# Optimization experiments

Hardware: AMD Instinct MI355X
Metric: run time of the kernel (lower is better)

## Reference

```python
import jax, jax.numpy as jnp
import numpy as np

N = 96        # num_nodes
D = 64        # emb_size / n_hid
BS = 16
T = 13
G = 1         # num_graph

# all N^2 ordered pairs, receiver-major: edge e=i*N+j has receiver i, sender j
_REC = jnp.repeat(jnp.arange(N), N)
_SEND = jnp.tile(jnp.arange(N), N)


def _lin(shape, key, scale=0.05):
    return (jax.random.normal(key, shape, dtype=jnp.float32) * scale)


def setup_inputs() -> dict:
    key = jax.random.key(0)
    ks = jax.random.split(key, 24)
    inp = {
        "skill_seq": jax.random.randint(ks[0], (BS, T), 0, N, dtype=jnp.int32),
        "adj": jax.random.uniform(ks[1], (G, BS, N, N), dtype=jnp.float32),
        "node_embeddings": jax.random.normal(ks[2], (G, N, D), dtype=jnp.float32),
        # edge MLP
        "W_msg1": _lin((2 * D, D), ks[3]), "b_msg1": jnp.zeros((D,), jnp.float32),
        "W_msg2": _lin((D, D), ks[4]),     "b_msg2": jnp.zeros((D,), jnp.float32),
        # GRU hidden projections (no bias)
        "W_hr": _lin((D, D), ks[5]), "W_hi": _lin((D, D), ks[6]), "W_hh": _lin((D, D), ks[7]),
        # GRU input projections (bias)
        "W_ir": _lin((D, D), ks[8]),  "b_ir": jnp.zeros((D,), jnp.float32),
        "W_ii": _lin((D, D), ks[9]),  "b_ii": jnp.zeros((D,), jnp.float32),
        "W_in": _lin((D, D), ks[10]), "b_in": jnp.zeros((D,), jnp.float32),
        # output MLP
        "W_o1": _lin((D, D), ks[11]), "b_o1": jnp.zeros((D,), jnp.float32),
        "W_o2": _lin((D, D), ks[12]), "b_o2": jnp.zeros((D,), jnp.float32),
        "W_o3": _lin((D, D), ks[13]), "b_o3": jnp.zeros((D,), jnp.float32),
    }
    return inp


def _forward(skill_seq, adj, node_embeddings,
             W_msg1, b_msg1, W_msg2, b_msg2,
             W_hr, W_hi, W_hh,
             W_ir, b_ir, W_ii, b_ii, W_in, b_in,
             W_o1, b_o1, W_o2, b_o2, W_o3, b_o3):
    bs, time_steps = skill_seq.shape
    hidden0 = jnp.zeros((G, bs, N, D), dtype=adj.dtype)
    emb = node_embeddings[0]  # [N, D] (num_graph=1)

    def step(hidden, skill_t):
        # gather senders/receivers over the node axis -> [G, bs, N^2, 2D]
        senders = hidden[:, :, _SEND, :]
        receivers = hidden[:, :, _REC, :]
        pre_msg = jnp.concatenate([senders, receivers], axis=-1)
        msg = jnp.tanh(pre_msg @ W_msg1 + b_msg1)        # [G, bs, N^2, D]
        msg = jnp.tanh(msg @ W_msg2 + b_msg2)
        msg = msg.reshape(G, bs, N, N, D)                # receiver i, sender j
        # mask by adjacency and scatter-sum over senders, then /N
        agg = jnp.einsum('gbij,gbijd->gbid', adj, msg) / N   # [G, bs, N, D]
        inputs = emb[skill_t][None, :, None, :]          # [1, bs, 1, D]
        r = jax.nn.sigmoid(inputs @ W_ir + b_ir + agg @ W_hr)
        i = jax.nn.sigmoid(inputs @ W_ii + b_ii + agg @ W_hi)
        n = jnp.tanh(inputs @ W_in + b_in + r * (agg @ W_hh))
        hidden = (1.0 - i) * n + i * hidden
        pred = jax.nn.relu(hidden @ W_o1 + b_o1)
        pred = jax.nn.relu(pred @ W_o2 + b_o2)
        pred = pred @ W_o3 + b_o3                        # [G, bs, N, D]
        return hidden, pred

    skills_t = skill_seq[:, :time_steps - 1].T           # [T-1, bs]
    _, preds = jax.lax.scan(step, hidden0, skills_t)     # [T-1, G, bs, N, D]
    # torch: stack(dim=1) -> [G, T-1, bs, N, D]; transpose(1,2) -> [G, bs, T-1, N, D]
    return jnp.transpose(preds, (1, 2, 0, 3, 4))


def reference(skill_seq, adj, node_embeddings,
              W_msg1, b_msg1, W_msg2, b_msg2,
              W_hr, W_hi, W_hh,
              W_ir, b_ir, W_ii, b_ii, W_in, b_in,
              W_o1, b_o1, W_o2, b_o2, W_o3, b_o3):
    return _forward(skill_seq, adj, node_embeddings,
                    W_msg1, b_msg1, W_msg2, b_msg2,
                    W_hr, W_hi, W_hh,
                    W_ir, b_ir, W_ii, b_ii, W_in, b_in,
                    W_o1, b_o1, W_o2, b_o2, W_o3, b_o3)
```

## Files before the change

### kernel.cpp

```cpp
#include <hip/hip_runtime.h>

typedef unsigned short ushort_t;
typedef __attribute__((ext_vector_type(8))) short short8;
typedef __attribute__((ext_vector_type(4))) float floatx4;

#define NN 96
#define DD 64
#define BSZ 16
#define TSTEP 12
#define JSPLIT 8
#define JPW 12
#define ITILES 6

#define OFF_HALL  0u
#define OFF_S     5111808u
#define OFF_R     5505024u
#define OFF_E     5898240u
#define OFF_PART  5971968u
#define OFF_WSWZ  9117696u
#define HSLOT     98304

static __device__ __forceinline__ short f2bf(float f){
    union { float f; unsigned u; } v; v.f = f;
    unsigned u = v.u;
    u += 0x7fffu + ((u >> 16) & 1u);
    return (short)(u >> 16);
}
static __device__ __forceinline__ float fast_tanh(float x){
    x = fminf(20.f, fmaxf(-20.f, x));
    float p = __expf(2.f * x);
    return (p - 1.f) * __builtin_amdgcn_rcpf(p + 1.f);
}
static __device__ __forceinline__ float fast_sigmoid(float x){
    x = fminf(30.f, fmaxf(-30.f, x));
    float p = __expf(-x);
    return __builtin_amdgcn_rcpf(1.f + p);
}
static __device__ __forceinline__ void zero4(floatx4* a){
    floatx4 z = {0.f,0.f,0.f,0.f};
    a[0]=z; a[1]=z; a[2]=z; a[3]=z;
}
static __device__ __forceinline__ void buildA(const float* sM, int col, int quad, short8& a0, short8& a1){
    floatx4 f0 = *(const floatx4*)&sM[col*68 + quad*8];
    floatx4 f1 = *(const floatx4*)&sM[col*68 + quad*8 + 4];
    floatx4 f2 = *(const floatx4*)&sM[col*68 + 32 + quad*8];
    floatx4 f3 = *(const floatx4*)&sM[col*68 + 32 + quad*8 + 4];
    #pragma unroll
    for (int jj = 0; jj < 4; jj++){
        a0[jj]   = f2bf(f0[jj]);
        a0[4+jj] = f2bf(f1[jj]);
        a1[jj]   = f2bf(f2[jj]);
        a1[4+jj] = f2bf(f3[jj]);
    }
}
static __device__ __forceinline__ void mm16(short8 a0, short8 a1, const short8* wzm, int l, floatx4* acc){
    #pragma unroll
    for (int nt = 0; nt < 4; nt++){
        short8 b0 = wzm[nt*64 + l];
        short8 b1 = wzm[(4 + nt)*64 + l];
        acc[nt] = __builtin_amdgcn_mfma_f32_16x16x32_bf16(a0, b0, acc[nt], 0, 0, 0);
        acc[nt] = __builtin_amdgcn_mfma_f32_16x16x32_bf16(a1, b1, acc[nt], 0, 0, 0);
    }
}
static __device__ __forceinline__ void mm16r(short8 a0, short8 a1, const short8* f, floatx4* acc){
    #pragma unroll
    for (int nt = 0; nt < 4; nt++){
        acc[nt] = __builtin_amdgcn_mfma_f32_16x16x32_bf16(a0, f[nt],     acc[nt], 0, 0, 0);
        acc[nt] = __builtin_amdgcn_mfma_f32_16x16x32_bf16(a1, f[4 + nt], acc[nt], 0, 0, 0);
    }
}

__global__ __launch_bounds__(256) void k_init(
    const float* __restrict__ emb, const float* __restrict__ Wmsg1,
    const float* __restrict__ Wmsg2,
    const float* __restrict__ Whr, const float* __restrict__ Whi, const float* __restrict__ Whh,
    const float* __restrict__ Wir, const float* __restrict__ bir,
    const float* __restrict__ Wii, const float* __restrict__ bii,
    const float* __restrict__ Win, const float* __restrict__ bin,
    const float* __restrict__ Wo1, const float* __restrict__ Wo2, const float* __restrict__ Wo3,
    float* __restrict__ hz, float* __restrict__ SRz,
    float* __restrict__ Ef, ushort_t* __restrict__ wswz)
{
    int wg = blockIdx.x, tid = threadIdx.x;
    if (wg < 288) {
        int flat = wg*256 + tid;
        floatx4 z = {0.f,0.f,0.f,0.f};
        if (flat < 24576) ((floatx4*)hz)[flat] = z;
        else              ((floatx4*)SRz)[flat - 24576] = z;
    } else if (wg < 360) {
        int flat = (wg - 288)*256 + tid;
        int m = flat / 6144; int r = flat % 6144; int s = r >> 6; int d = r & 63;
        const float* W = (m==0)? Wir : (m==1)? Wii : Win;
        const float* B = (m==0)? bir : (m==1)? bii : bin;
        float acc = B[d];
        #pragma unroll 8
        for (int k = 0; k < 64; k++)
            acc += emb[s*64 + k] * W[k*64 + d];
        Ef[flat] = acc;
    } else {
        int flat = (wg - 360)*256 + tid;
        int m = flat >> 12; int q = flat & 4095;
        int jj = q & 7, lane = (q >> 3) & 63, nt = (q >> 9) & 3, kc = q >> 11;
        int k = kc*32 + ((lane >> 4) << 3) + jj;
        int n = nt*16 + (lane & 15);
        const float* src; int idx = k*64 + n;
        switch (m) {
          case 0: src = Wmsg2; break;
          case 1: src = Whr;  break;
          case 2: src = Whi;  break;
          case 3: src = Whh;  break;
          case 4: src = Wmsg1; break;
          case 5: src = Wmsg1; idx = (64 + k)*64 + n; break;
          case 6: src = Wo1; break;
          case 7: src = Wo2; break;
          default: src = Wo3; break;
        }
        wswz[flat] = (ushort_t)f2bf(src[idx]);
    }
}

__global__ __launch_bounds__(256) void k_msg(
    const float* __restrict__ adj, const float* __restrict__ b1in, const float* __restrict__ b2in,
    const float* __restrict__ Sg, const float* __restrict__ Rg,
    const ushort_t* __restrict__ wswz, float* __restrict__ partial)
{
    __shared__ float sS[JPW*64];
    __shared__ float sRB[16*68];
    __shared__ float sAdj[16*JPW];
    __shared__ float sAgg[4][16*68];
    int wg = blockIdx.x;
    int js = wg / 96; int rem = wg % 96; int b = rem / 6; int it = rem % 6;
    int tid = threadIdx.x; int w = tid >> 6; int l = tid & 63;
    int quad = l >> 4, col = l & 15;
    int j0 = js * JPW;

    for (int q = tid; q < JPW*16; q += 256) {
        int row = q >> 4, c4 = (q & 15) * 4;
        *(floatx4*)&sS[row*64 + c4] = *(const floatx4*)&Sg[(b*NN + j0 + row)*64 + c4];
    }
    for (int q = tid; q < 16*16; q += 256) {
        int row = q >> 4, c4 = (q & 15) * 4;
        floatx4 r4 = *(const floatx4*)&Rg[(b*NN + it*16 + row)*64 + c4];
        floatx4 b4 = *(const floatx4*)&b1in[c4];
        floatx4 o = r4 + b4;
        *(floatx4*)&sRB[row*68 + c4] = o;
    }
    for (int q = tid; q < 16*JPW; q += 256) {
        int i = q / JPW, j = q % JPW;
        sAdj[q] = adj[(b*NN + it*16 + i)*NN + j0 + j];
    }
    const short8* wz = (const short8*)wswz;
    short8 w2f[2][4];
    #pragma unroll
    for (int kc = 0; kc < 2; kc++)
      #pragma unroll
      for (int nt = 0; nt < 4; nt++)
        w2f[kc][nt] = wz[(kc*4 + nt)*64 + l];
    float b2v[4];
    #pragma unroll
    for (int nt = 0; nt < 4; nt++) b2v[nt] = b2in[nt*16 + col];
    __syncthreads();

    float rbv[16];
    #pragma unroll
    for (int c = 0; c < 4; c++)
        *(floatx4*)&rbv[c*4] = *(const floatx4*)&sRB[col*68 + (c>>1)*32 + quad*8 + (c&1)*4];

    float agg[4][4];
    #pragma unroll
    for (int nt=0;nt<4;nt++)
      #pragma unroll
      for (int r=0;r<4;r++) agg[nt][r] = 0.f;

    for (int c = 0; c < 3; c++) {
        int jl = w*3 + c;
        float sv[16];
        #pragma unroll
        for (int cc = 0; cc < 4; cc++)
            *(floatx4*)&sv[cc*4] = *(const floatx4*)&sS[jl*64 + (cc>>1)*32 + quad*8 + (cc&1)*4];
        short8 a0, a1;
        #pragma unroll
        for (int e = 0; e < 8; e++) {
            a0[e] = f2bf(fast_tanh(sv[e]   + rbv[e]));
            a1[e] = f2bf(fast_tanh(sv[8+e] + rbv[8+e]));
        }
        floatx4 acc[4];
        zero4(acc);
        #pragma unroll
        for (int nt = 0; nt < 4; nt++) {
            acc[nt] = __builtin_amdgcn_mfma_f32_16x16x32_bf16(a0, w2f[0][nt], acc[nt], 0,0,0);
            acc[nt] = __builtin_amdgcn_mfma_f32_16x16x32_bf16(a1, w2f[1][nt], acc[nt], 0,0,0);
        }
        float adjv[4];
        #pragma unroll
        for (int r = 0; r < 4; r++) adjv[r] = sAdj[(quad*4 + r)*JPW + jl];
        #pragma unroll
        for (int nt = 0; nt < 4; nt++)
          #pragma unroll
          for (int r = 0; r < 4; r++)
            agg[nt][r] += adjv[r] * fast_tanh(acc[nt][r] + b2v[nt]);
    }
    #pragma unroll
    for (int nt = 0; nt < 4; nt++)
      #pragma unroll
      for (int r = 0; r < 4; r++)
        sAgg[w][(quad*4 + r)*68 + nt*16 + col] = agg[nt][r];
    __syncthreads();
    {
        int i = tid >> 4, k4 = (tid & 15) * 4;
        floatx4 s0 = *(const floatx4*)&sAgg[0][i*68 + k4];
        floatx4 s1 = *(const floatx4*)&sAgg[1][i*68 + k4];
        floatx4 s2 = *(const floatx4*)&sAgg[2][i*68 + k4];
        floatx4 s3 = *(const floatx4*)&sAgg[3][i*68 + k4];
        floatx4 o = (s0 + s1) + (s2 + s3);
        o = o * (1.f/96.f);
        *(floatx4*)&partial[((js*BSZ + b)*NN + it*16 + i)*64 + k4] = o;
    }
}

__global__ __launch_bounds__(256) void k_gru(
    const int* __restrict__ skills, const float* __restrict__ partial,
    const float* __restrict__ Ef, const ushort_t* __restrict__ wswz,
    const float* __restrict__ hprev, float* __restrict__ hcur,
    float* __restrict__ Sg, float* __restrict__ Rg, int t)
{
    __shared__ float sM[16*68];
    __shared__ float sG[3][16*68];
    __shared__ float sH[16*64];
    __shared__ float sE[3][64];
    int wg = blockIdx.x; int b = wg / 6, it = wg % 6;
    int tid = threadIdx.x; int w = tid >> 6; int l = tid & 63;
    int quad = l >> 4, col = l & 15;
    int i = tid >> 4, k4 = (tid & 15) * 4;

    const short8* wzb = (const short8*)wswz;
    short8 fG[8], fSR[8];
    if (w < 3) {
        #pragma unroll
        for (int q = 0; q < 8; q++) fG[q] = wzb[(1 + w)*512 + q*64 + l];
    }
    if (w < 2) {
        #pragma unroll
        for (int q = 0; q < 8; q++) fSR[q] = wzb[(4 + w)*512 + q*64 + l];
    }

    {
        floatx4 a = {0.f,0.f,0.f,0.f};
        #pragma unroll
        for (int p = 0; p < JSPLIT; p++)
            a += *(const floatx4*)&partial[((p*BSZ + b)*NN + it*16 + i)*64 + k4];
        *(floatx4*)&sM[i*68 + k4] = a;
        *(floatx4*)&sH[i*64 + k4] = *(const floatx4*)&hprev[(b*NN + it*16 + i)*64 + k4];
    }
    if (tid < 192) {
        int s = skills[b*13 + t];
        ((float*)sE)[tid] = Ef[(tid >> 6)*6144 + s*64 + (tid & 63)];
    }
    __syncthreads();

    if (w < 3) {
        short8 a0, a1;
        buildA(sM, col, quad, a0, a1);
        floatx4 acc[4];
        zero4(acc);
        mm16r(a0, a1, fG, acc);
        #pragma unroll
        for (int nt = 0; nt < 4; nt++)
          #pragma unroll
          for (int r = 0; r < 4; r++)
            sG[w][(quad*4 + r)*68 + nt*16 + col] = acc[nt][r];
    }
    __syncthreads();

    {
        float h[4];
        #pragma unroll
        for (int e = 0; e < 4; e++) {
            int d = k4 + e;
            float gr = fast_sigmoid(sE[0][d] + sG[0][i*68 + d]);
            float gi = fast_sigmoid(sE[1][d] + sG[1][i*68 + d]);
            float nv = fast_tanh(sE[2][d] + gr * sG[2][i*68 + d]);
            h[e] = (1.f - gi)*nv + gi*sH[i*64 + d];
        }
        #pragma unroll
        for (int e = 0; e < 4; e++) sM[i*68 + k4 + e] = h[e];
        floatx4 hv = { h[0], h[1], h[2], h[3] };
        *(floatx4*)&hcur[(b*NN + it*16 + i)*64 + k4] = hv;
    }
    __syncthreads();

    if (w < 2) {
        short8 a0, a1;
        buildA(sM, col, quad, a0, a1);
        floatx4 acc[4];
        zero4(acc);
        mm16r(a0, a1, fSR, acc);
        float* dst = (w == 0) ? Sg : Rg;
        #pragma unroll
        for (int nt = 0; nt < 4; nt++)
          #pragma unroll
          for (int r = 0; r < 4; r++)
            dst[(b*NN + it*16 + quad*4 + r)*64 + nt*16 + col] = acc[nt][r];
    }
}

__global__ __launch_bounds__(256) void k_out(
    const float* __restrict__ hall, const ushort_t* __restrict__ wswz,
    const float* __restrict__ bo1, const float* __restrict__ bo2, const float* __restrict__ bo3,
    float* __restrict__ out)
{
    __shared__ float sT[4][16*68];
    int tid = threadIdx.x; int w = tid >> 6; int l = tid & 63;
    int quad = l >> 4, col = l & 15;
    int g = blockIdx.x*4 + w;
    int ts = g / 96; int rem = g % 96; int b = rem / 6, it = rem % 6;
    const float* hsrc = hall + (size_t)(ts + 1)*HSLOT + (b*NN + it*16)*64;
    float* sm = sT[w];
    {
        int i = l >> 2, c0 = (l & 3) * 16;
        #pragma unroll
        for (int cc = 0; cc < 4; cc++)
            *(floatx4*)&sm[i*68 + c0 + cc*4] = *(const floatx4*)&hsrc[i*64 + c0 + cc*4];
    }
    float bv1[4], bv2[4], bv3[4];
    #pragma unroll
    for (int nt = 0; nt < 4; nt++) {
        bv1[nt] = bo1[nt*16 + col];
        bv2[nt] = bo2[nt*16 + col];
        bv3[nt] = bo3[nt*16 + col];
    }
    short8 a0, a1;
    floatx4 acc[4];

    buildA(sm, col, quad, a0, a1);
    zero4(acc);
    mm16(a0, a1, (const short8*)wswz + 6*512, l, acc);
    #pragma unroll
    for (int nt = 0; nt < 4; nt++)
      #pragma unroll
      for (int r = 0; r < 4; r++)
        sm[(quad*4 + r)*68 + nt*16 + col] = fmaxf(0.f, acc[nt][r] + bv1[nt]);

    buildA(sm, col, quad, a0, a1);
    zero4(acc);
    mm16(a0, a1, (const short8*)wswz + 7*512, l, acc);
    #pragma unroll
    for (int nt = 0; nt < 4; nt++)
      #pragma unroll
      for (int r = 0; r < 4; r++)
        sm[(quad*4 + r)*68 + nt*16 + col] = fmaxf(0.f, acc[nt][r] + bv2[nt]);

    buildA(sm, col, quad, a0, a1);
    zero4(acc);
    mm16(a0, a1, (const short8*)wswz + 8*512, l, acc);
    #pragma unroll
    for (int nt = 0; nt < 4; nt++)
      #pragma unroll
      for (int r = 0; r < 4; r++)
        out[((b*TSTEP + ts)*NN + it*16 + quad*4 + r)*64 + nt*16 + col] = acc[nt][r] + bv3[nt];
}

extern "C" void kernel_launch(void* const* d_in, const int* in_sizes, int n_in,
                              void* d_out, int out_size, void* d_ws, size_t ws_size,
                              hipStream_t stream) {
    const int*   skills = (const int*)d_in[0];
    const float* adj    = (const float*)d_in[1];
    const float* emb    = (const float*)d_in[2];
    const float* Wmsg1  = (const float*)d_in[3];
    const float* b1     = (const float*)d_in[4];
    const float* Wmsg2  = (const float*)d_in[5];
    const float* b2     = (const float*)d_in[6];
    const float* Whr    = (const float*)d_in[7];
    const float* Whi    = (const float*)d_in[8];
    const float* Whh    = (const float*)d_in[9];
    const float* Wir    = (const float*)d_in[10];
    const float* bir    = (const float*)d_in[11];
    const float* Wii    = (const float*)d_in[12];
    const float* bii    = (const float*)d_in[13];
    const float* Win    = (const float*)d_in[14];
    const float* bin    = (const float*)d_in[15];
    const float* Wo1    = (const float*)d_in[16];
    const float* bo1    = (const float*)d_in[17];
    const float* Wo2    = (const float*)d_in[18];
    const float* bo2    = (const float*)d_in[19];
    const float* Wo3    = (const float*)d_in[20];
    const float* bo3    = (const float*)d_in[21];

    char* ws = (char*)d_ws;
    float*    hall    = (float*)(ws + OFF_HALL);
    float*    Sg      = (float*)(ws + OFF_S);
    float*    Rg      = (float*)(ws + OFF_R);
    float*    Ef      = (float*)(ws + OFF_E);
    float*    partial = (float*)(ws + OFF_PART);
    ushort_t* wswz    = (ushort_t*)(ws + OFF_WSWZ);
    float*    out     = (float*)d_out;

    k_init<<<dim3(504), dim3(256), 0, stream>>>(emb, Wmsg1, Wmsg2, Whr, Whi, Whh,
        Wir, bir, Wii, bii, Win, bin, Wo1, Wo2, Wo3, hall, Sg, Ef, wswz);

    for (int t = 0; t < TSTEP; t++) {
        k_msg<<<dim3(JSPLIT*BSZ*ITILES), dim3(256), 0, stream>>>(adj, b1, b2, Sg, Rg, wswz, partial);
        k_gru<<<dim3(BSZ*ITILES), dim3(256), 0, stream>>>(skills, partial, Ef, wswz,
            hall + (size_t)t*HSLOT, hall + (size_t)(t+1)*HSLOT, Sg, Rg, t);
    }
    k_out<<<dim3(288), dim3(256), 0, stream>>>(hall, wswz, bo1, bo2, bo3, out);
}
```

Measured before the change: 273.5 us.

## Fuse final GRU step into output kernel, rebalance msg split, use native bf16 casts

The last timestep's GRU update now runs inside k_out for the final slot, which removes one k_gru launch and its dependent h write/read. The message kernel's j-split goes from 8 to 12 with 8 senders per workgroup, and its inner loop is fully unrolled, trading more partial-sum traffic for more parallel workgroups. Manual float-to-bf16 rounding is replaced by native __bf16 conversions, and the clamps in tanh and sigmoid are dropped. Removing the clamps risks inf/NaN for large arguments, because the exp-based formulas can overflow to inf/inf.

```diff
diff --git a/kernel.cpp b/kernel.cpp
--- a/kernel.cpp
+++ b/kernel.cpp
@@ -2,14 +2,15 @@
 
 typedef unsigned short ushort_t;
 typedef __attribute__((ext_vector_type(8))) short short8;
+typedef __attribute__((ext_vector_type(8))) __bf16 bf16x8;
 typedef __attribute__((ext_vector_type(4))) float floatx4;
 
 #define NN 96
 #define DD 64
 #define BSZ 16
 #define TSTEP 12
-#define JSPLIT 8
-#define JPW 12
+#define JSPLIT 12
+#define JPW 8
 #define ITILES 6
 
 #define OFF_HALL  0u
@@ -17,8 +18,10 @@
 #define OFF_R     5505024u
 #define OFF_E     5898240u
 #define OFF_PART  5971968u
-#define OFF_WSWZ  9117696u
+#define OFF_WSWZ  10690560u
 #define HSLOT     98304
+
+union fragU { short8 s; bf16x8 b; };
 
 static __device__ __forceinline__ short f2bf(float f){
     union { float f; unsigned u; } v; v.f = f;
@@ -27,12 +30,10 @@
     return (short)(u >> 16);
 }
 static __device__ __forceinline__ float fast_tanh(float x){
-    x = fminf(20.f, fmaxf(-20.f, x));
     float p = __expf(2.f * x);
     return (p - 1.f) * __builtin_amdgcn_rcpf(p + 1.f);
 }
 static __device__ __forceinline__ float fast_sigmoid(float x){
-    x = fminf(30.f, fmaxf(-30.f, x));
     float p = __expf(-x);
     return __builtin_amdgcn_rcpf(1.f + p);
 }
@@ -45,13 +46,15 @@
     floatx4 f1 = *(const floatx4*)&sM[col*68 + quad*8 + 4];
     floatx4 f2 = *(const floatx4*)&sM[col*68 + 32 + quad*8];
     floatx4 f3 = *(const floatx4*)&sM[col*68 + 32 + quad*8 + 4];
+    fragU u0, u1;
     #pragma unroll
     for (int jj = 0; jj < 4; jj++){
-        a0[jj]   = f2bf(f0[jj]);
-        a0[4+jj] = f2bf(f1[jj]);
-        a1[jj]   = f2bf(f2[jj]);
-        a1[4+jj] = f2bf(f3[jj]);
-    }
+        u0.b[jj]   = (__bf16)f0[jj];
+        u0.b[4+jj] = (__bf16)f1[jj];
+        u1.b[jj]   = (__bf16)f2[jj];
+        u1.b[4+jj] = (__bf16)f3[jj];
+    }
+    a0 = u0.s; a1 = u1.s;
 }
 static __device__ __forceinline__ void mm16(short8 a0, short8 a1, const short8* wzm, int l, floatx4* acc){
     #pragma unroll
@@ -78,15 +81,16 @@
     const float* __restrict__ Wii, const float* __restrict__ bii,
     const float* __restrict__ Win, const float* __restrict__ bin,
     const float* __restrict__ Wo1, const float* __restrict__ Wo2, const float* __restrict__ Wo3,
-    float* __restrict__ hz, float* __restrict__ SRz,
+    float* __restrict__ hz, float* __restrict__ S0, float* __restrict__ R0,
     float* __restrict__ Ef, ushort_t* __restrict__ wswz)
 {
     int wg = blockIdx.x, tid = threadIdx.x;
     if (wg < 288) {
         int flat = wg*256 + tid;
         floatx4 z = {0.f,0.f,0.f,0.f};
-        if (flat < 24576) ((floatx4*)hz)[flat] = z;
-        else              ((floatx4*)SRz)[flat - 24576] = z;
+        if      (flat < 24576) ((floatx4*)hz)[flat] = z;
+        else if (flat < 49152) ((floatx4*)S0)[flat - 24576] = z;
+        else                   ((floatx4*)R0)[flat - 49152] = z;
     } else if (wg < 360) {
         int flat = (wg - 288)*256 + tid;
         int m = flat / 6144; int r = flat % 6144; int s = r >> 6; int d = r & 63;
@@ -172,24 +176,25 @@
       #pragma unroll
       for (int r=0;r<4;r++) agg[nt][r] = 0.f;
 
-    for (int c = 0; c < 3; c++) {
-        int jl = w*3 + c;
+    #pragma unroll
+    for (int c = 0; c < 2; c++) {
+        int jl = w*2 + c;
         float sv[16];
         #pragma unroll
         for (int cc = 0; cc < 4; cc++)
             *(floatx4*)&sv[cc*4] = *(const floatx4*)&sS[jl*64 + (cc>>1)*32 + quad*8 + (cc&1)*4];
-        short8 a0, a1;
+        fragU u0, u1;
         #pragma unroll
         for (int e = 0; e < 8; e++) {
-            a0[e] = f2bf(fast_tanh(sv[e]   + rbv[e]));
-            a1[e] = f2bf(fast_tanh(sv[8+e] + rbv[8+e]));
+            u0.b[e] = (__bf16)fast_tanh(sv[e]   + rbv[e]);
+            u1.b[e] = (__bf16)fast_tanh(sv[8+e] + rbv[8+e]);
         }
         floatx4 acc[4];
         zero4(acc);
         #pragma unroll
         for (int nt = 0; nt < 4; nt++) {
-            acc[nt] = __builtin_amdgcn_mfma_f32_16x16x32_bf16(a0, w2f[0][nt], acc[nt], 0,0,0);
-            acc[nt] = __builtin_amdgcn_mfma_f32_16x16x32_bf16(a1, w2f[1][nt], acc[nt], 0,0,0);
+            acc[nt] = __builtin_amdgcn_mfma_f32_16x16x32_bf16(u0.s, w2f[0][nt], acc[nt], 0,0,0);
+            acc[nt] = __builtin_amdgcn_mfma_f32_16x16x32_bf16(u1.s, w2f[1][nt], acc[nt], 0,0,0);
         }
         float adjv[4];
         #pragma unroll
@@ -305,7 +310,9 @@
 }
 
 __global__ __launch_bounds__(256) void k_out(
-    const float* __restrict__ hall, const ushort_t* __restrict__ wswz,
+    const int* __restrict__ skills, const float* __restrict__ partial,
+    const float* __restrict__ Ef, const float* __restrict__ hall,
+    const ushort_t* __restrict__ wswz,
     const float* __restrict__ bo1, const float* __restrict__ bo2, const float* __restrict__ bo3,
     float* __restrict__ out)
 {
@@ -314,14 +321,50 @@
     int quad = l >> 4, col = l & 15;
     int g = blockIdx.x*4 + w;
     int ts = g / 96; int rem = g % 96; int b = rem / 6, it = rem % 6;
-    const float* hsrc = hall + (size_t)(ts + 1)*HSLOT + (b*NN + it*16)*64;
     float* sm = sT[w];
-    {
-        int i = l >> 2, c0 = (l & 3) * 16;
+
+    if (ts < 11) {
+        const float* hsrc = hall + (size_t)(ts + 1)*HSLOT + (b*NN + it*16)*64;
+        int i = l >> 2, c0 = (l & 3)*16;
         #pragma unroll
         for (int cc = 0; cc < 4; cc++)
             *(floatx4*)&sm[i*68 + c0 + cc*4] = *(const floatx4*)&hsrc[i*64 + c0 + cc*4];
-    }
+    } else {
+        int i = l >> 2, c0 = (l & 3)*16;
+        floatx4 a[4]; zero4(a);
+        for (int p = 0; p < JSPLIT; p++) {
+            const float* base = &partial[((p*BSZ + b)*NN + it*16 + i)*64 + c0];
+            #pragma unroll
+            for (int cc = 0; cc < 4; cc++) a[cc] += *(const floatx4*)&base[cc*4];
+        }
+        #pragma unroll
+        for (int cc = 0; cc < 4; cc++) *(floatx4*)&sm[i*68 + c0 + cc*4] = a[cc];
+
+        short8 a0, a1; buildA(sm, col, quad, a0, a1);
+        floatx4 Ar[4], Ai[4], Ah[4];
+        zero4(Ar); zero4(Ai); zero4(Ah);
+        mm16(a0, a1, (const short8*)wswz + 1*512, l, Ar);
+        mm16(a0, a1, (const short8*)wswz + 2*512, l, Ai);
+        mm16(a0, a1, (const short8*)wswz + 3*512, l, Ah);
+        int s = skills[b*13 + 11];
+        const float* hp = hall + 11*(size_t)HSLOT;
+        #pragma unroll
+        for (int nt = 0; nt < 4; nt++) {
+            int d = nt*16 + col;
+            float er = Ef[0*6144 + s*64 + d];
+            float ei = Ef[1*6144 + s*64 + d];
+            float en = Ef[2*6144 + s*64 + d];
+            #pragma unroll
+            for (int r = 0; r < 4; r++) {
+                int row = it*16 + quad*4 + r;
+                float gr = fast_sigmoid(er + Ar[nt][r]);
+                float gi = fast_sigmoid(ei + Ai[nt][r]);
+                float nv = fast_tanh  (en + gr*Ah[nt][r]);
+                sm[(quad*4 + r)*68 + d] = (1.f - gi)*nv + gi*hp[(b*NN + row)*64 + d];
+            }
+        }
+    }
+
     float bv1[4], bv2[4], bv3[4];
     #pragma unroll
     for (int nt = 0; nt < 4; nt++) {
@@ -396,12 +439,14 @@
     float*    out     = (float*)d_out;
 
     k_init<<<dim3(504), dim3(256), 0, stream>>>(emb, Wmsg1, Wmsg2, Whr, Whi, Whh,
-        Wir, bir, Wii, bii, Win, bin, Wo1, Wo2, Wo3, hall, Sg, Ef, wswz);
+        Wir, bir, Wii, bii, Win, bin, Wo1, Wo2, Wo3, hall, Sg, Rg, Ef, wswz);
 
     for (int t = 0; t < TSTEP; t++) {
         k_msg<<<dim3(JSPLIT*BSZ*ITILES), dim3(256), 0, stream>>>(adj, b1, b2, Sg, Rg, wswz, partial);
-        k_gru<<<dim3(BSZ*ITILES), dim3(256), 0, stream>>>(skills, partial, Ef, wswz,
-            hall + (size_t)t*HSLOT, hall + (size_t)(t+1)*HSLOT, Sg, Rg, t);
-    }
-    k_out<<<dim3(288), dim3(256), 0, stream>>>(hall, wswz, bo1, bo2, bo3, out);
-}
+        if (t < TSTEP - 1)
+            k_gru<<<dim3(BSZ*ITILES), dim3(256), 0, stream>>>(skills, partial, Ef, wswz,
+                hall + (size_t)t*HSLOT, hall + (size_t)(t+1)*HSLOT, Sg, Rg, t);
+    }
+    k_out<<<dim3(288), dim3(256), 0, stream>>>(skills, partial, Ef, hall, wswz,
+        bo1, bo2, bo3, out);
+}
```

Result: no change. 272.3 us (-0.4%).
